# Kernel tuning notes

Measured on AMD Instinct MI355X. Metric: run time of the kernel, lower is better.

## Reference

```python
import jax, jax.numpy as jnp
import numpy as np

N_EMBD = 2048
N_HEAD = 16
D_HEAD = N_EMBD // N_HEAD


def setup_inputs() -> dict:
    key = jax.random.key(0)
    k1, k2, k3 = jax.random.split(key, 3)
    x = jax.random.normal(k1, (2, 2048, N_EMBD), dtype=jnp.float32)
    # torch Linear stores weight as [out, in]; kept in that layout
    w_qkv = jax.random.normal(k2, (3 * N_EMBD, N_EMBD), dtype=jnp.float32) * (1.0 / np.sqrt(N_EMBD))
    w_out = jax.random.normal(k3, (N_EMBD, N_EMBD), dtype=jnp.float32) * (1.0 / np.sqrt(N_EMBD))
    return {"x": x, "w_qkv": w_qkv, "w_out": w_out}


def reference(x, w_qkv, w_out):
    B, T, C = x.shape
    H, D = N_HEAD, D_HEAD
    qkv = jnp.einsum('btc,oc->bto', x, w_qkv)            # [B,T,3C]
    qkv = qkv.reshape(B, T, 3, H, D)
    q = jnp.transpose(qkv[:, :, 0], (0, 2, 1, 3))        # [B,H,T,D]
    k = jnp.transpose(qkv[:, :, 1], (0, 2, 1, 3))
    v = jnp.transpose(qkv[:, :, 2], (0, 2, 1, 3))
    scale = 1.0 / np.sqrt(D).astype(np.float32)
    att = jnp.einsum('bhqd,bhkd->bhqk', q, k) * scale    # [B,H,T,T]
    causal = jnp.tril(jnp.ones((T, T), dtype=bool))
    att = jnp.where(causal[None, None], att, jnp.finfo(att.dtype).min)
    att = jax.nn.softmax(att, axis=-1)
    y = jnp.einsum('bhqk,bhkd->bhqd', att, v)            # [B,H,T,D]
    y = jnp.transpose(y, (0, 2, 1, 3)).reshape(B, T, C)
    return jnp.einsum('btc,oc->bto', y, w_out)
```

## Files before the change

kernel.cpp:

```cpp
#include <hip/hip_runtime.h>
#include <stdint.h>


typedef __attribute__((ext_vector_type(8))) short bf16x8;
typedef __attribute__((ext_vector_type(8))) unsigned short u16x8;
typedef __attribute__((ext_vector_type(4))) unsigned short u16x4;
typedef __attribute__((ext_vector_type(4))) float f32x4;

#define MFMA16(a, b, c) __builtin_amdgcn_mfma_f32_16x16x32_bf16((a), (b), (c), 0, 0, 0)

__device__ __forceinline__ unsigned short f2bf(float f) {
  union { float f; uint32_t u; } v; v.f = f;
  uint32_t r = v.u + 0x7FFFu + ((v.u >> 16) & 1u);
  return (unsigned short)(r >> 16);
}

__device__ __forceinline__ void gld_lds16(const unsigned short* g, unsigned short* lds) {
  __builtin_amdgcn_global_load_lds(
      (const __attribute__((address_space(1))) void*)g,
      (__attribute__((address_space(3))) void*)lds, 16, 0, 0);
}

__device__ __forceinline__ void cvt8(const float* __restrict__ in,
                                     unsigned short* __restrict__ out, int i) {
  float4 a = reinterpret_cast<const float4*>(in)[i * 2];
  float4 b = reinterpret_cast<const float4*>(in)[i * 2 + 1];
  u16x8 o;
  o[0] = f2bf(a.x); o[1] = f2bf(a.y); o[2] = f2bf(a.z); o[3] = f2bf(a.w);
  o[4] = f2bf(b.x); o[5] = f2bf(b.y); o[6] = f2bf(b.z); o[7] = f2bf(b.w);
  reinterpret_cast<u16x8*>(out)[i] = o;
}

__global__ __launch_bounds__(256) void cvt_all(const float* __restrict__ x,
                                               const float* __restrict__ wq,
                                               const float* __restrict__ wo,
                                               unsigned short* __restrict__ xb,
                                               unsigned short* __restrict__ wqb,
                                               unsigned short* __restrict__ wob) {
  const int stride = gridDim.x * blockDim.x;
  const int t0 = blockIdx.x * blockDim.x + threadIdx.x;
  for (int i = t0; i < 1048576; i += stride) cvt8(x, xb, i);
  for (int i = t0; i < 1572864; i += stride) cvt8(wq, wqb, i);
  for (int i = t0; i < 524288; i += stride) cvt8(wo, wob, i);
}

__device__ __forceinline__ void gemm128_core(const unsigned short* __restrict__ A,
                                             const unsigned short* __restrict__ Bt,
                                             int K, int brow, int bcol,
                                             unsigned short* lds_a, unsigned short* lds_b,
                                             f32x4 acc[4][4]) {
  const int tid = threadIdx.x;
  const int l   = tid & 63;
  const int w   = tid >> 6;
  const int wr  = (w >> 1) << 6;
  const int wc  = (w & 1) << 6;

  const int srow = tid >> 2;
  const int sswz = (tid & 3) ^ ((srow >> 1) & 3);
  const unsigned short* gA0 = A  + (size_t)(brow + srow) * K + 8 * sswz;
  const unsigned short* gA1 = gA0 + (size_t)64 * K;
  const unsigned short* gB0 = Bt + (size_t)(bcol + srow) * K + 8 * sswz;
  const unsigned short* gB1 = gB0 + (size_t)64 * K;

  unsigned short* la0 = lds_a + tid * 8;
  unsigned short* la1 = lds_a + (256 + tid) * 8;
  unsigned short* lb0 = lds_b + tid * 8;
  unsigned short* lb1 = lds_b + (256 + tid) * 8;

  const int fm    = l & 15;
  const int fswz8 = 8 * ((l >> 4) ^ ((fm >> 1) & 3));

  for (int k0 = 0; k0 < K; k0 += 32) {
    gld_lds16(gA0, la0);
    gld_lds16(gA1, la1);
    gld_lds16(gB0, lb0);
    gld_lds16(gB1, lb1);
    gA0 += 32; gA1 += 32; gB0 += 32; gB1 += 32;
    __syncthreads();
    bf16x8 af[4], bfv[4];
#pragma unroll
    for (int i = 0; i < 4; i++)
      af[i] = *(const bf16x8*)&lds_a[(wr + i * 16 + fm) * 32 + fswz8];
#pragma unroll
    for (int j = 0; j < 4; j++)
      bfv[j] = *(const bf16x8*)&lds_b[(wc + j * 16 + fm) * 32 + fswz8];
#pragma unroll
    for (int i = 0; i < 4; i++)
#pragma unroll
      for (int j = 0; j < 4; j++)
        acc[i][j] = MFMA16(af[i], bfv[j], acc[i][j]);
    __syncthreads();
  }
}

__global__ __launch_bounds__(256) void gemm_qkv(const unsigned short* __restrict__ xb,
                                                const unsigned short* __restrict__ wqb,
                                                unsigned short* __restrict__ Qb,
                                                unsigned short* __restrict__ Kb,
                                                unsigned short* __restrict__ Vtb) {
  __shared__ alignas(16) unsigned short lds_a[128 * 32];
  __shared__ alignas(16) unsigned short lds_b[128 * 32];
  f32x4 acc[4][4];
#pragma unroll
  for (int i = 0; i < 4; i++)
#pragma unroll
    for (int j = 0; j < 4; j++) acc[i][j] = (f32x4){0.f, 0.f, 0.f, 0.f};

  const int brow = blockIdx.y << 7;
  const int bcol = blockIdx.x << 7;
  gemm128_core(xb, wqb, 2048, brow, bcol, lds_a, lds_b, acc);

  const int l = threadIdx.x & 63;
  const int w = threadIdx.x >> 6;
  const int wr = (w >> 1) << 6, wc = (w & 1) << 6;
  const int which = bcol >> 11;
  const int bh = ((brow >> 11) << 4) | ((bcol >> 7) & 15);
  const int tbase = (brow & 2047) + wr + ((l >> 4) << 2);

#pragma unroll
  for (int i = 0; i < 4; i++) {
    const int t0 = tbase + i * 16;
#pragma unroll
    for (int j = 0; j < 4; j++) {
      const int d = wc + j * 16 + (l & 15);
      if (which == 2) {
        u16x4 pk;
#pragma unroll
        for (int r = 0; r < 4; r++) pk[r] = f2bf(acc[i][j][r]);
        *reinterpret_cast<u16x4*>(&Vtb[((size_t)bh * 128 + d) * 2048 + t0]) = pk;
      } else {
        unsigned short* dst = (which == 0 ? Qb : Kb) + ((size_t)bh * 2048 + t0) * 128 + d;
#pragma unroll
        for (int r = 0; r < 4; r++) dst[(size_t)r * 128] = f2bf(acc[i][j][r]);
      }
    }
  }
}

__global__ __launch_bounds__(256) void gemm_out(const unsigned short* __restrict__ yb,
                                                const unsigned short* __restrict__ wob,
                                                float* __restrict__ out) {
  __shared__ alignas(16) unsigned short lds_a[128 * 32];
  __shared__ alignas(16) unsigned short lds_b[128 * 32];
  f32x4 acc[4][4];
#pragma unroll
  for (int i = 0; i < 4; i++)
#pragma unroll
    for (int j = 0; j < 4; j++) acc[i][j] = (f32x4){0.f, 0.f, 0.f, 0.f};

  const int brow = blockIdx.y << 7;
  const int bcol = blockIdx.x << 7;
  gemm128_core(yb, wob, 2048, brow, bcol, lds_a, lds_b, acc);

  const int l = threadIdx.x & 63;
  const int w = threadIdx.x >> 6;
  const int wr = (w >> 1) << 6, wc = (w & 1) << 6;
#pragma unroll
  for (int i = 0; i < 4; i++) {
    const int m0 = brow + wr + i * 16 + ((l >> 4) << 2);
#pragma unroll
    for (int j = 0; j < 4; j++) {
      const int n = bcol + wc + j * 16 + (l & 15);
#pragma unroll
      for (int r = 0; r < 4; r++) out[(size_t)(m0 + r) * 2048 + n] = acc[i][j][r];
    }
  }
}

__device__ __forceinline__ void stage_kv64(const unsigned short* __restrict__ Kg,
                                           const unsigned short* __restrict__ Vg,
                                           int kv0, unsigned short* dk,
                                           unsigned short* dv, int tid) {
#pragma unroll
  for (int c = 0; c < 2; c++) {
    int s = c * 512 + tid;
    int row = s >> 4, g = s & 15;
    gld_lds16(&Kg[(size_t)(kv0 + row) * 128 + 8 * (g ^ (row & 7))], &dk[s * 8]);
  }
#pragma unroll
  for (int c = 0; c < 2; c++) {
    int s = c * 512 + tid;
    int row = s >> 3, g = s & 7;
    gld_lds16(&Vg[(size_t)row * 2048 + kv0 + 8 * (g ^ (row & 7))], &dv[s * 8]);
  }
}

__device__ __forceinline__ void attn_tile_step(const bf16x8 qf[4], f32x4 yacc[8],
                                               float mrow[4], float lsum[4],
                                               int qw0, int kv0,
                                               const unsigned short* kb,
                                               const unsigned short* vb,
                                               unsigned short* pw, int l) {
  const float SC = 0.12752585f;
  f32x4 sfr[4];
  __builtin_amdgcn_s_setprio(1);
#pragma unroll
  for (int kt = 0; kt < 4; kt++) {
    const int kr = kt * 16 + (l & 15);
    f32x4 s4 = (f32x4){0.f, 0.f, 0.f, 0.f};
#pragma unroll
    for (int ds = 0; ds < 4; ds++) {
      bf16x8 kfr = *(const bf16x8*)&kb[kr * 128 + 8 * (((ds << 2) + (l >> 4)) ^ (kr & 7))];
      s4 = MFMA16(qf[ds], kfr, s4);
    }
    sfr[kt] = s4;
  }
  __builtin_amdgcn_s_setprio(0);
  const bool need_mask = (kv0 + 63 > qw0);
#pragma unroll
  for (int kt = 0; kt < 4; kt++)
#pragma unroll
    for (int r = 0; r < 4; r++) {
      float sv = sfr[kt][r] * SC;
      if (need_mask) {
        int qa = qw0 + ((l >> 4) << 2) + r;
        int ka = kv0 + kt * 16 + (l & 15);
        sv = (ka > qa) ? -1e30f : sv;
      }
      sfr[kt][r] = sv;
    }
  float prmax[4];
#pragma unroll
  for (int r = 0; r < 4; r++)
    prmax[r] = fmaxf(fmaxf(sfr[0][r], sfr[1][r]), fmaxf(sfr[2][r], sfr[3][r]));
  bool sm = (prmax[0] <= mrow[0] + 8.f) && (prmax[1] <= mrow[1] + 8.f) &&
            (prmax[2] <= mrow[2] + 8.f) && (prmax[3] <= mrow[3] + 8.f);
  if (!__all(sm)) {
    float f[4];
#pragma unroll
    for (int r = 0; r < 4; r++) {
      float m = prmax[r];
      m = fmaxf(m, __shfl_xor(m, 1));
      m = fmaxf(m, __shfl_xor(m, 2));
      m = fmaxf(m, __shfl_xor(m, 4));
      m = fmaxf(m, __shfl_xor(m, 8));
      float mn = fmaxf(mrow[r], m);
      f[r] = exp2f(mrow[r] - mn);
      mrow[r] = mn;
      lsum[r] *= f[r];
    }
#pragma unroll
    for (int dt = 0; dt < 8; dt++)
#pragma unroll
      for (int r = 0; r < 4; r++) yacc[dt][r] *= f[r];
  }
#pragma unroll
  for (int kt = 0; kt < 4; kt++)
#pragma unroll
    for (int r = 0; r < 4; r++) {
      float p = exp2f(sfr[kt][r] - mrow[r]);
      lsum[r] += p;
      int row = ((l >> 4) << 2) + r;
      int k = kt * 16 + (l & 15);
      pw[row * 64 + (((k >> 3) ^ (row & 7)) << 3) + (k & 7)] = f2bf(p);
    }
  asm volatile("s_waitcnt lgkmcnt(0)" ::: "memory");
  __builtin_amdgcn_sched_barrier(0);
  __builtin_amdgcn_s_setprio(1);
#pragma unroll
  for (int ks = 0; ks < 2; ks++) {
    const int prow = l & 15;
    bf16x8 pa = *(const bf16x8*)&pw[prow * 64 + ((((ks << 2) + (l >> 4)) ^ (prow & 7)) << 3)];
#pragma unroll
    for (int dt = 0; dt < 8; dt++) {
      const int d = dt * 16 + (l & 15);
      bf16x8 vv = *(const bf16x8*)&vb[d * 64 + ((((ks << 2) + (l >> 4)) ^ (d & 7)) << 3)];
      yacc[dt] = MFMA16(pa, vv, yacc[dt]);
    }
  }
  __builtin_amdgcn_s_setprio(0);
}

__global__ __launch_bounds__(512, 4) void attn_kernel(const unsigned short* __restrict__ Qb,
                                                      const unsigned short* __restrict__ Kb,
                                                      const unsigned short* __restrict__ Vtb,
                                                      unsigned short* __restrict__ Yb) {
  __shared__ alignas(16) unsigned short lds_k[2][64 * 128];
  __shared__ alignas(16) unsigned short lds_v[2][128 * 64];
  __shared__ alignas(16) unsigned short p_lds[8][16 * 64];

  const int tid = threadIdx.x;
  const int l = tid & 63;
  const int w = tid >> 6;

  const int bid = blockIdx.x;
  const int xcd = bid & 7;
  const int loc = bid >> 3;
  const int bh = xcd * 4 + (loc >> 4);
  const int jraw = loc & 15;
  const int jidx = (loc < 32) ? jraw : (15 - jraw);

  const int b = bh >> 4, h = bh & 15;

  const unsigned short* Qg = Qb + (size_t)bh * 2048 * 128;
  const unsigned short* Kg = Kb + (size_t)bh * 2048 * 128;
  const unsigned short* Vg = Vtb + (size_t)bh * 128 * 2048;

  const int my_j = (w < 4) ? jidx : (31 - jidx);
  const int qw0 = (my_j << 6) + ((w & 3) << 4);

  bf16x8 qf[4];
#pragma unroll
  for (int ds = 0; ds < 4; ds++)
    qf[ds] = *(const bf16x8*)&Qg[(size_t)(qw0 + (l & 15)) * 128 + ds * 32 + 8 * (l >> 4)];

  f32x4 yacc[8];
#pragma unroll
  for (int dt = 0; dt < 8; dt++) yacc[dt] = (f32x4){0.f, 0.f, 0.f, 0.f};
  float mrow[4], lsum[4];
#pragma unroll
  for (int r = 0; r < 4; r++) { mrow[r] = -1e30f; lsum[r] = 0.f; }

  const int nkv = (31 - jidx) + 1;

  stage_kv64(Kg, Vg, 0, lds_k[0], lds_v[0], tid);
  asm volatile("s_waitcnt vmcnt(0)" ::: "memory");
  __syncthreads();

  for (int t = 0; t < nkv; t++) {
    const int kv0 = t << 6;
    const int buf = t & 1;
    if (t + 1 < nkv)
      stage_kv64(Kg, Vg, kv0 + 64, lds_k[buf ^ 1], lds_v[buf ^ 1], tid);

    if (kv0 <= qw0 + 15)
      attn_tile_step(qf, yacc, mrow, lsum, qw0, kv0, lds_k[buf], lds_v[buf],
                     p_lds[w], l);

    asm volatile("s_waitcnt vmcnt(0)" ::: "memory");
    __syncthreads();
  }

  float lrow[4];
#pragma unroll
  for (int r = 0; r < 4; r++) {
    float s = lsum[r];
    s += __shfl_xor(s, 1); s += __shfl_xor(s, 2);
    s += __shfl_xor(s, 4); s += __shfl_xor(s, 8);
    lrow[r] = s;
  }
#pragma unroll
  for (int dt = 0; dt < 8; dt++)
#pragma unroll
    for (int r = 0; r < 4; r++) {
      int qa = qw0 + ((l >> 4) << 2) + r;
      Yb[((size_t)(b * 2048 + qa)) * 2048 + h * 128 + dt * 16 + (l & 15)] =
          f2bf(yacc[dt][r] / lrow[r]);
    }
}

extern "C" void kernel_launch(void* const* d_in, const int* in_sizes, int n_in,
                              void* d_out, int out_size, void* d_ws, size_t ws_size,
                              hipStream_t stream) {
  const float* x    = (const float*)d_in[0];
  const float* wqkv = (const float*)d_in[1];
  const float* wout = (const float*)d_in[2];
  float* out = (float*)d_out;

  unsigned short* ws  = (unsigned short*)d_ws;
  unsigned short* xb  = ws;
  unsigned short* wqb = xb + (size_t)8388608;
  unsigned short* wob = wqb + (size_t)12582912;
  unsigned short* Qb  = wob + (size_t)4194304;
  unsigned short* Kb  = Qb + (size_t)8388608;
  unsigned short* Vtb = Kb + (size_t)8388608;
  unsigned short* Yb  = Vtb + (size_t)8388608;

  cvt_all<<<2048, 256, 0, stream>>>(x, wqkv, wout, xb, wqb, wob);
  gemm_qkv<<<dim3(48, 32), 256, 0, stream>>>(xb, wqb, Qb, Kb, Vtb);
  attn_kernel<<<512, 512, 0, stream>>>(Qb, Kb, Vtb, Yb);
  gemm_out<<<dim3(16, 32), 256, 0, stream>>>(Yb, wob, out);
}
```

Measured before the change: 262.3 us.

## Deepen GEMM K-tile to 64, fold softmax scale into Q, truncate P to bf16

The shared GEMM core now stages a 64-wide K slice per iteration with an 8-way XOR swizzle, halving the number of barrier pairs and loop iterations per tile at the cost of twice the LDS per block. The softmax scale (including log2e) is folded into Q during the QKV GEMM epilogue, which removes a multiply per score element in the attention inner loop and leaves masking to boundary tiles only. The P probabilities are converted to bf16 by truncation instead of round-to-nearest, trading a small accuracy loss for fewer ALU ops.

```diff
diff --git a/kernel.cpp b/kernel.cpp
--- a/kernel.cpp
+++ b/kernel.cpp
@@ -55,40 +55,40 @@
   const int wr  = (w >> 1) << 6;
   const int wc  = (w & 1) << 6;
 
-  const int srow = tid >> 2;
-  const int sswz = (tid & 3) ^ ((srow >> 1) & 3);
-  const unsigned short* gA0 = A  + (size_t)(brow + srow) * K + 8 * sswz;
-  const unsigned short* gA1 = gA0 + (size_t)64 * K;
-  const unsigned short* gB0 = Bt + (size_t)(bcol + srow) * K + 8 * sswz;
-  const unsigned short* gB1 = gB0 + (size_t)64 * K;
-
-  unsigned short* la0 = lds_a + tid * 8;
-  unsigned short* la1 = lds_a + (256 + tid) * 8;
-  unsigned short* lb0 = lds_b + tid * 8;
-  unsigned short* lb1 = lds_b + (256 + tid) * 8;
-
-  const int fm    = l & 15;
-  const int fswz8 = 8 * ((l >> 4) ^ ((fm >> 1) & 3));
-
-  for (int k0 = 0; k0 < K; k0 += 32) {
-    gld_lds16(gA0, la0);
-    gld_lds16(gA1, la1);
-    gld_lds16(gB0, lb0);
-    gld_lds16(gB1, lb1);
-    gA0 += 32; gA1 += 32; gB0 += 32; gB1 += 32;
+  const int srow = tid >> 3;
+  const int gsrc = (tid & 7) ^ (srow & 7);
+  const unsigned short* gA0 = A  + (size_t)(brow + srow) * K + 8 * gsrc;
+  const unsigned short* gB0 = Bt + (size_t)(bcol + srow) * K + 8 * gsrc;
+  unsigned short* dA0 = lds_a + tid * 8;
+  unsigned short* dB0 = lds_b + tid * 8;
+
+  const int fm = l & 15;
+  const int q  = l >> 4;
+
+  for (int k0 = 0; k0 < K; k0 += 64) {
+#pragma unroll
+    for (int c = 0; c < 4; c++)
+      gld_lds16(gA0 + (size_t)c * 32 * K + k0, dA0 + c * 2048);
+#pragma unroll
+    for (int c = 0; c < 4; c++)
+      gld_lds16(gB0 + (size_t)c * 32 * K + k0, dB0 + c * 2048);
     __syncthreads();
-    bf16x8 af[4], bfv[4];
-#pragma unroll
-    for (int i = 0; i < 4; i++)
-      af[i] = *(const bf16x8*)&lds_a[(wr + i * 16 + fm) * 32 + fswz8];
-#pragma unroll
-    for (int j = 0; j < 4; j++)
-      bfv[j] = *(const bf16x8*)&lds_b[(wc + j * 16 + fm) * 32 + fswz8];
-#pragma unroll
-    for (int i = 0; i < 4; i++)
+#pragma unroll
+    for (int ks = 0; ks < 2; ks++) {
+      const int goff = 8 * ((ks * 4 + q) ^ (fm & 7));
+      bf16x8 af[4], bfv[4];
+#pragma unroll
+      for (int i = 0; i < 4; i++)
+        af[i] = *(const bf16x8*)&lds_a[(wr + i * 16 + fm) * 64 + goff];
 #pragma unroll
       for (int j = 0; j < 4; j++)
-        acc[i][j] = MFMA16(af[i], bfv[j], acc[i][j]);
+        bfv[j] = *(const bf16x8*)&lds_b[(wc + j * 16 + fm) * 64 + goff];
+#pragma unroll
+      for (int i = 0; i < 4; i++)
+#pragma unroll
+        for (int j = 0; j < 4; j++)
+          acc[i][j] = MFMA16(af[i], bfv[j], acc[i][j]);
+    }
     __syncthreads();
   }
 }
@@ -98,8 +98,8 @@
                                                 unsigned short* __restrict__ Qb,
                                                 unsigned short* __restrict__ Kb,
                                                 unsigned short* __restrict__ Vtb) {
-  __shared__ alignas(16) unsigned short lds_a[128 * 32];
-  __shared__ alignas(16) unsigned short lds_b[128 * 32];
+  __shared__ alignas(16) unsigned short lds_a[128 * 64];
+  __shared__ alignas(16) unsigned short lds_b[128 * 64];
   f32x4 acc[4][4];
 #pragma unroll
   for (int i = 0; i < 4; i++)
@@ -114,6 +114,7 @@
   const int w = threadIdx.x >> 6;
   const int wr = (w >> 1) << 6, wc = (w & 1) << 6;
   const int which = bcol >> 11;
+  const float qs = (which == 0) ? 0.12752585f : 1.0f;
   const int bh = ((brow >> 11) << 4) | ((bcol >> 7) & 15);
   const int tbase = (brow & 2047) + wr + ((l >> 4) << 2);
 
@@ -131,7 +132,7 @@
       } else {
         unsigned short* dst = (which == 0 ? Qb : Kb) + ((size_t)bh * 2048 + t0) * 128 + d;
 #pragma unroll
-        for (int r = 0; r < 4; r++) dst[(size_t)r * 128] = f2bf(acc[i][j][r]);
+        for (int r = 0; r < 4; r++) dst[(size_t)r * 128] = f2bf(acc[i][j][r] * qs);
       }
     }
   }
@@ -140,8 +141,8 @@
 __global__ __launch_bounds__(256) void gemm_out(const unsigned short* __restrict__ yb,
                                                 const unsigned short* __restrict__ wob,
                                                 float* __restrict__ out) {
-  __shared__ alignas(16) unsigned short lds_a[128 * 32];
-  __shared__ alignas(16) unsigned short lds_b[128 * 32];
+  __shared__ alignas(16) unsigned short lds_a[128 * 64];
+  __shared__ alignas(16) unsigned short lds_b[128 * 64];
   f32x4 acc[4][4];
 #pragma unroll
   for (int i = 0; i < 4; i++)
@@ -191,7 +192,6 @@
                                                const unsigned short* kb,
                                                const unsigned short* vb,
                                                unsigned short* pw, int l) {
-  const float SC = 0.12752585f;
   f32x4 sfr[4];
   __builtin_amdgcn_s_setprio(1);
 #pragma unroll
@@ -207,18 +207,16 @@
   }
   __builtin_amdgcn_s_setprio(0);
   const bool need_mask = (kv0 + 63 > qw0);
-#pragma unroll
-  for (int kt = 0; kt < 4; kt++)
-#pragma unroll
-    for (int r = 0; r < 4; r++) {
-      float sv = sfr[kt][r] * SC;
-      if (need_mask) {
+  if (need_mask) {
+#pragma unroll
+    for (int kt = 0; kt < 4; kt++)
+#pragma unroll
+      for (int r = 0; r < 4; r++) {
         int qa = qw0 + ((l >> 4) << 2) + r;
         int ka = kv0 + kt * 16 + (l & 15);
-        sv = (ka > qa) ? -1e30f : sv;
+        if (ka > qa) sfr[kt][r] = -1e30f;
       }
-      sfr[kt][r] = sv;
-    }
+  }
   float prmax[4];
 #pragma unroll
   for (int r = 0; r < 4; r++)
@@ -250,9 +248,11 @@
     for (int r = 0; r < 4; r++) {
       float p = exp2f(sfr[kt][r] - mrow[r]);
       lsum[r] += p;
+      union { float f; uint32_t u; } cc; cc.f = p;
       int row = ((l >> 4) << 2) + r;
       int k = kt * 16 + (l & 15);
-      pw[row * 64 + (((k >> 3) ^ (row & 7)) << 3) + (k & 7)] = f2bf(p);
+      pw[row * 64 + (((k >> 3) ^ (row & 7)) << 3) + (k & 7)] =
+          (unsigned short)(cc.u >> 16);
     }
   asm volatile("s_waitcnt lgkmcnt(0)" ::: "memory");
   __builtin_amdgcn_sched_barrier(0);
```

New measurement: 246.4 us. -6.1%, faster.
